# Performance work log

Hardware: AMD Instinct MI355X
Metric: run time of the kernel (lower is better)

Reference implementation:

```python
import jax, jax.numpy as jnp
import numpy as np
import math

N = 8192
F_IN = 1024
F_OUT = 1024
MAX_ITER = 10


def whale_optimizer(positions, key, max_iter=MAX_ITER):
    """Vectorized whale optimization algorithm.

    Faithful to the original per-agent/per-dim update rules, but the agent
    loop is vectorized (on-device RNG, one parallel update per outer
    iteration); only the `max_iter` outer iterations stay sequential.
    positions: [N, D] float32.
    """
    n, d = positions.shape
    lower = jnp.min(positions)
    upper = jnp.max(positions)
    k0, loop_key = jax.random.split(key)
    leader = positions[jax.random.randint(k0, (), 0, n)]  # [D]

    def step(carry, it):
        pos, leader = carry
        itf = it.astype(jnp.float32)
        k = jax.random.fold_in(loop_key, it)
        k1, k2, k3, k4, k5, k6 = jax.random.split(k, 6)
        a = 2.0 - itf * (2.0 / max_iter)
        a2 = -1.0 + itf * (-1.0 / max_iter)
        r1 = jax.random.uniform(k1, (n, 1))
        r2 = jax.random.uniform(k2, (n, 1))
        A = 2.0 * a * r1 - a                       # [n,1]
        C = 2.0 * r2                               # [n,1]
        lp = (a2 - 1.0) * jax.random.uniform(k3, (n, 1)) + 1.0  # spiral param
        p = jax.random.uniform(k4, (n, 1))
        # random leader per (agent, dim), as in the original inner j-loop
        ridx = jax.random.randint(k5, (n, d), 0, n)
        x_rand = jnp.take_along_axis(pos, ridx, axis=0)         # [n,d]
        explore = jnp.abs(x_rand - A * jnp.abs(C * x_rand - pos))
        exploit = jnp.abs(leader - A * jnp.abs(C * leader - pos))
        spiral = jnp.abs(jnp.abs(leader - pos) * jnp.exp(lp) * jnp.cos(2.0 * jnp.pi * lp) + leader)
        new_pos = jnp.where(p < 0.5,
                            jnp.where(jnp.abs(A) >= 1.0, explore, exploit),
                            spiral)
        new_pos = jnp.clip(new_pos, lower, upper)
        new_leader = new_pos[jax.random.randint(k6, (), 0, n)]
        return (new_pos, new_leader), None

    (positions, _), _ = jax.lax.scan(step, (positions, leader), jnp.arange(max_iter))
    return positions


def setup_inputs() -> dict:
    key = jax.random.key(0)
    k1, k2, k3, k4 = jax.random.split(key, 4)
    stdv = 1.0 / math.sqrt(F_OUT)
    return {
        "input": jax.random.normal(k1, (N, F_IN), dtype=jnp.float32),
        "adj": jax.random.uniform(k2, (N, N), dtype=jnp.float32) * (1.0 / N),
        "h0": jax.random.normal(k3, (N, F_IN), dtype=jnp.float32),
        "weight": jax.random.uniform(k4, (F_IN, F_OUT), dtype=jnp.float32,
                                      minval=-stdv, maxval=stdv),
        "lamda": jnp.float32(0.5),
        "alpha": jnp.float32(0.1),
        "l": 1,
    }


def reference(input, adj, h0, weight, lamda, alpha, l):
    # variant=False, residual=False
    theta = jnp.log(lamda / l + 1.0)
    hi = adj @ input                                  # spmm(adj, input)
    support = (1.0 - alpha) * hi + alpha * h0
    r = support
    # original detaches support before the whale optimizer
    opt = whale_optimizer(jax.lax.stop_gradient(support), jax.random.key(42))
    output = theta * (opt @ weight) + (1.0 - theta) * r
    return output
```

## Files before the change

### kernel.cpp

```cpp
#include <hip/hip_runtime.h>
#include <hip/hip_bf16.h>
#include <stdint.h>
#include <math.h>

typedef uint32_t u32;
typedef __hip_bfloat16 bf16t;
typedef __attribute__((ext_vector_type(8))) short short8;
typedef __attribute__((ext_vector_type(4))) float f32x4;


__host__ __device__ __forceinline__ void tf2(u32 k0, u32 k1, u32 c0, u32 c1, u32& o0, u32& o1) {
  const u32 ks2 = k0 ^ k1 ^ 0x1BD11BDAu;
  u32 x0 = c0 + k0, x1 = c1 + k1;
#define TFROT(v,r) (((v)<<(r))|((v)>>(32-(r))))
#define TFR(r) { x0 += x1; x1 = TFROT(x1,r); x1 ^= x0; }
  TFR(13) TFR(15) TFR(26) TFR(6)   x0 += k1;  x1 += ks2 + 1u;
  TFR(17) TFR(29) TFR(16) TFR(24)  x0 += ks2; x1 += k0 + 2u;
  TFR(13) TFR(15) TFR(26) TFR(6)   x0 += k0;  x1 += k1 + 3u;
  TFR(17) TFR(29) TFR(16) TFR(24)  x0 += k1;  x1 += ks2 + 4u;
  TFR(13) TFR(15) TFR(26) TFR(6)   x0 += ks2; x1 += k0 + 5u;
#undef TFR
#undef TFROT
  o0 = x0; o1 = x1;
}

__device__ __forceinline__ float unif_row(u32 ka, u32 kb, int i) {
  u32 o0, o1;
  tf2(ka, kb, 0u, (u32)i, o0, o1);
  return __uint_as_float(0x3F800000u | ((o0 ^ o1) >> 9)) - 1.0f;
}

__device__ __forceinline__ int ridx_fn(u32 ka, u32 kb, u32 f) {
  u32 o0, o1; tf2(ka, kb, 0u, f, o0, o1); return (int)((o0 ^ o1) & 8191u);
}

static inline void split2(u32 ka, u32 kb, u32* kA, u32* kB) {
  u32 a0, a1, b0, b1;
  tf2(ka, kb, 0u, 0u, a0, a1);
  tf2(ka, kb, 0u, 1u, b0, b1);
  kA[0] = a0; kA[1] = a1; kB[0] = b0; kB[1] = b1;
}

static inline void split6(u32 ka, u32 kb, u32 out[6][2]) {
  for (u32 i = 0; i < 6; i++) { u32 o0, o1; tf2(ka, kb, 0u, i, o0, o1); out[i][0] = o0; out[i][1] = o1; }
}

static inline int scalar_randint8192(u32 ka, u32 kb) {
  u32 kA[2], kB[2];
  split2(ka, kb, kA, kB);
  u32 o0, o1;
  tf2(kB[0], kB[1], 0u, 0u, o0, o1);
  return (int)((o0 ^ o1) & 8191u);
}

__device__ __forceinline__ ushort f2bf(float f) {
  u32 u = __float_as_uint(f);
  u32 r = u + 0x7FFFu + ((u >> 16) & 1u);
  return (ushort)(r >> 16);
}

__global__ __launch_bounds__(256) void cvt_k(const float4* __restrict__ x, uint2* __restrict__ y, int n4) {
  for (int i = blockIdx.x * 256 + threadIdx.x; i < n4; i += gridDim.x * 256) {
    float4 v = x[i];
    uint2 o;
    o.x = (u32)f2bf(v.x) | ((u32)f2bf(v.y) << 16);
    o.y = (u32)f2bf(v.z) | ((u32)f2bf(v.w) << 16);
    y[i] = o;
  }
}

__global__ __launch_bounds__(256) void packb_k(const float* __restrict__ B, uint4* __restrict__ out, int K, int Nn) {
  const int idx = blockIdx.x * 256 + threadIdx.x;
  const int total = (K >> 3) * Nn;
  if (idx >= total) return;
  const int g = idx / Nn;
  const int n = idx - g * Nn;
  u32 wv[4];
#pragma unroll
  for (int j = 0; j < 4; j++) {
    const float f0 = B[(size_t)(g * 8 + 2 * j) * Nn + n];
    const float f1 = B[(size_t)(g * 8 + 2 * j + 1) * Nn + n];
    wv[j] = (u32)f2bf(f0) | ((u32)f2bf(f1) << 16);
  }
  uint4 o; o.x = wv[0]; o.y = wv[1]; o.z = wv[2]; o.w = wv[3];
  out[idx] = o;
}

__global__ __launch_bounds__(256) void minmax2_k(const float* __restrict__ part, int G, float* __restrict__ bnd) {
  __shared__ float slo[256], shi[256];
  const int tid = threadIdx.x;
  float lo = 3.4e38f, hi = -3.4e38f;
  for (int i = tid; i < G; i += 256) { lo = fminf(lo, part[i]); hi = fmaxf(hi, part[G + i]); }
  slo[tid] = lo; shi[tid] = hi; __syncthreads();
  for (int s = 128; s > 0; s >>= 1) {
    if (tid < s) { slo[tid] = fminf(slo[tid], slo[tid + s]); shi[tid] = fmaxf(shi[tid], shi[tid + s]); }
    __syncthreads();
  }
  if (tid == 0) { bnd[0] = slo[0]; bnd[1] = shi[0]; }
}

__device__ __forceinline__ void gld_lds16(const void* g, void* l) {
  __builtin_amdgcn_global_load_lds((const __attribute__((address_space(1))) void*)g,
                                   (__attribute__((address_space(3))) void*)l, 16, 0, 0);
}

template <int EPI>
__global__ __launch_bounds__(512, 4) void gemm_k(
    const bf16t* __restrict__ A, const bf16t* __restrict__ Bp,
    const float* __restrict__ aux, const float* __restrict__ sF,
    const int* __restrict__ sI, float* __restrict__ C,
    float* __restrict__ prt, int PG, int Nn, int K) {
  __shared__ __align__(16) bf16t As[128 * 32];
  __shared__ __align__(16) bf16t Bs[128 * 32];
  const int tid = threadIdx.x;
  const int lane = tid & 63;
  const int wave = tid >> 6;
  const int bm = blockIdx.x & 63;
  const int bn = blockIdx.x >> 6;
  const int m0 = bm << 7, n0 = bn << 7;
  const int wm = (wave & 1) << 6;
  const int wn = (wave >> 1) << 5;

  f32x4 acc[4][2];
#pragma unroll
  for (int i = 0; i < 4; i++)
#pragma unroll
    for (int j = 0; j < 2; j++) acc[i][j] = (f32x4){0.f, 0.f, 0.f, 0.f};

  const bf16t* gA = A + (size_t)(m0 + (tid >> 2)) * K + ((tid & 3) << 3);
  bf16t* lA = As + (tid << 3);
  const bf16t* gB = Bp + ((size_t)(tid >> 7) * Nn + n0 + (tid & 127)) * 8;
  bf16t* lB = Bs + (tid << 3);
  const size_t bstep = (size_t)Nn * 32;

  for (int k0 = 0; k0 < K; k0 += 32) {
    __syncthreads();
    gld_lds16(gA + k0, lA);
    gld_lds16(gB, lB);
    gB += bstep;
    __syncthreads();
    const int arow = lane & 15, aq = lane >> 4;
    short8 af[4], bfv[2];
#pragma unroll
    for (int mt = 0; mt < 4; mt++)
      af[mt] = *(const short8*)(As + ((wm + mt * 16 + arow) << 5) + (aq << 3));
#pragma unroll
    for (int nt = 0; nt < 2; nt++)
      bfv[nt] = *(const short8*)(Bs + (((aq << 7) + wn + nt * 16 + arow) << 3));
#pragma unroll
    for (int mt = 0; mt < 4; mt++)
#pragma unroll
      for (int nt = 0; nt < 2; nt++)
        acc[mt][nt] = __builtin_amdgcn_mfma_f32_16x16x32_bf16(af[mt], bfv[nt], acc[mt][nt], 0, 0, 0);
  }

  float p1, p2;
  if (EPI == 1) { const float al = sF[0]; p1 = 1.0f - al; p2 = al; }
  else { const float th = logf(sF[0] / (float)sI[0] + 1.0f); p1 = th; p2 = 1.0f - th; }
  const int col = lane & 15, rq = lane >> 4;
  float vlo = 3.4e38f, vhi = -3.4e38f;
#pragma unroll
  for (int mt = 0; mt < 4; mt++)
#pragma unroll
    for (int nt = 0; nt < 2; nt++)
#pragma unroll
      for (int r = 0; r < 4; r++) {
        const int gm = m0 + wm + mt * 16 + (rq << 2) + r;
        const int gn = n0 + wn + nt * 16 + col;
        const size_t ix = (size_t)gm * Nn + gn;
        const float v = p1 * acc[mt][nt][r] + p2 * aux[ix];
        C[ix] = v;
        if (EPI == 1) { vlo = fminf(vlo, v); vhi = fmaxf(vhi, v); }
      }
  if (EPI == 1) {
    __syncthreads();
    float* red = (float*)As;
    red[tid] = vlo; red[512 + tid] = vhi;
    __syncthreads();
    for (int s = 256; s > 0; s >>= 1) {
      if (tid < s) {
        red[tid] = fminf(red[tid], red[tid + s]);
        red[512 + tid] = fmaxf(red[512 + tid], red[512 + tid + s]);
      }
      __syncthreads();
    }
    if (tid == 0) { prt[blockIdx.x] = red[0]; prt[PG + blockIdx.x] = red[512]; }
  }
}

struct WA {
  u32 k1a, k1b, k2a, k2b, k3a, k3b, k4a, k4b, k5a, k5b;
  int ldr;
  float a, a2;
};

__global__ __launch_bounds__(256) void whale_k(
    const float* __restrict__ pinb, float* __restrict__ poutb,
    ushort* __restrict__ opt, const float* __restrict__ bnd, WA w) {
  const int row = blockIdx.x;
  const int tid = threadIdx.x;
  __shared__ float sh[4];
  if (tid < 4) {
    u32 ka, kb;
    if (tid == 0)      { ka = w.k1a; kb = w.k1b; }
    else if (tid == 1) { ka = w.k2a; kb = w.k2b; }
    else if (tid == 2) { ka = w.k3a; kb = w.k3b; }
    else               { ka = w.k4a; kb = w.k4b; }
    sh[tid] = unif_row(ka, kb, row);
  }
  __syncthreads();
  const float r1 = sh[0], r2 = sh[1], u3 = sh[2], p = sh[3];
  float t2 = (2.0f * w.a) * r1;
  asm volatile("" : "+v"(t2));
  const float A = t2 - w.a;
  const float Cc = 2.0f * r2;
  const float lo = bnd[0], hi = bnd[1];
  const float* pin = pinb + ((size_t)row << 10);
  const int j0 = tid << 2;
  float4 pv = *(const float4*)(pin + j0);
  float ov[4];
  const bool bp = (p < 0.5f);
  if (bp && (fabsf(A) >= 1.0f)) {
    const u32 fb = ((u32)row << 10) + (u32)j0;
#pragma unroll
    for (int e = 0; e < 4; e++) {
      const float pos = (&pv.x)[e];
      const int ri = ridx_fn(w.k5a, w.k5b, fb + (u32)e);
      const float xr = pinb[((size_t)ri << 10) + j0 + e];
      ov[e] = fabsf(xr - A * fabsf(Cc * xr - pos));
    }
  } else {
    const float* ldp = pinb + ((size_t)w.ldr << 10);
    float4 lv = *(const float4*)(ldp + j0);
    if (bp) {
#pragma unroll
      for (int e = 0; e < 4; e++) {
        const float pos = (&pv.x)[e], ld = (&lv.x)[e];
        ov[e] = fabsf(ld - A * fabsf(Cc * ld - pos));
      }
    } else {
      const float lp = (w.a2 - 1.0f) * u3 + 1.0f;
      const float s1 = expf(lp);
      const float s2 = cosf(6.2831855f * lp);
#pragma unroll
      for (int e = 0; e < 4; e++) {
        const float pos = (&pv.x)[e], ld = (&lv.x)[e];
        ov[e] = fabsf(fabsf(ld - pos) * s1 * s2 + ld);
      }
    }
  }
  float4 res;
#pragma unroll
  for (int e = 0; e < 4; e++) (&res.x)[e] = fminf(fmaxf(ov[e], lo), hi);
  *(float4*)(poutb + ((size_t)row << 10) + j0) = res;
  if (opt) {
    ushort4 o4;
    o4.x = f2bf(res.x); o4.y = f2bf(res.y); o4.z = f2bf(res.z); o4.w = f2bf(res.w);
    *(ushort4*)(opt + ((size_t)row << 10) + j0) = o4;
  }
}

extern "C" void kernel_launch(void* const* d_in, const int* in_sizes, int n_in,
                              void* d_out, int out_size, void* d_ws, size_t ws_size,
                              hipStream_t stream) {
  const float* inp = (const float*)d_in[0];
  const float* adj = (const float*)d_in[1];
  const float* h0  = (const float*)d_in[2];
  const float* wgt = (const float*)d_in[3];
  const float* lam = (const float*)d_in[4];
  const float* alp = (const float*)d_in[5];
  const int* lint  = (const int*)d_in[6];
  float* outp = (float*)d_out;

  char* ws = (char*)d_ws;
  bf16t* Abf  = (bf16t*)(ws);
  float* P0   = (float*)(ws);
  float* P1   = (float*)(ws + 33554432);
  ushort* OPT = (ushort*)(ws + 67108864);
  bf16t* B1p  = (bf16t*)(ws + 134217728);
  bf16t* Wp   = (bf16t*)(ws + 150994944);
  float* SUP  = (float*)(ws + 153092096);
  float* PRT  = (float*)(ws + 186646528);
  float* BND  = (float*)(ws + 186662912);

  hipLaunchKernelGGL(cvt_k, dim3(4096), dim3(256), 0, stream, (const float4*)adj, (uint2*)Abf, 16777216);
  hipLaunchKernelGGL(packb_k, dim3(4096), dim3(256), 0, stream, inp, (uint4*)B1p, 8192, 1024);
  hipLaunchKernelGGL(packb_k, dim3(512), dim3(256), 0, stream, wgt, (uint4*)Wp, 1024, 1024);
  hipLaunchKernelGGL((gemm_k<1>), dim3(512), dim3(512), 0, stream, Abf, B1p, h0, alp, lint, SUP, PRT, 512, 1024, 8192);
  hipLaunchKernelGGL(minmax2_k, dim3(1), dim3(256), 0, stream, PRT, 512, BND);

  u32 k0k[2], lpk[2];
  split2(0u, 42u, k0k, lpk);
  int ldr = scalar_randint8192(k0k[0], k0k[1]);
  const float* cur = SUP;
  float* bufs[2] = {P0, P1};
  for (int it = 0; it < 10; ++it) {
    u32 ka, kb; tf2(lpk[0], lpk[1], 0u, (u32)it, ka, kb);
    u32 ks[6][2];
    split6(ka, kb, ks);
    u32 k5A[2], k5B[2];
    split2(ks[4][0], ks[4][1], k5A, k5B);
    WA w;
    w.k1a = ks[0][0]; w.k1b = ks[0][1];
    w.k2a = ks[1][0]; w.k2b = ks[1][1];
    w.k3a = ks[2][0]; w.k3b = ks[2][1];
    w.k4a = ks[3][0]; w.k4b = ks[3][1];
    w.k5a = k5B[0];   w.k5b = k5B[1];
    w.ldr = ldr;
    const float itf = (float)it;
    w.a = 2.0f - itf * 0.2f;
    w.a2 = -1.0f + itf * (-0.1f);
    float* nxt = bufs[it & 1];
    hipLaunchKernelGGL(whale_k, dim3(8192), dim3(256), 0, stream, cur, nxt,
                       (it == 9) ? OPT : (ushort*)nullptr, BND, w);
    cur = nxt;
    ldr = scalar_randint8192(ks[5][0], ks[5][1]);
  }
  hipLaunchKernelGGL((gemm_k<2>), dim3(512), dim3(512), 0, stream, (const bf16t*)OPT, Wp, SUP, lam, lint, outp,
                     (float*)nullptr, 0, 1024, 1024);
  (void)in_sizes; (void)n_in; (void)out_size; (void)ws_size;
}
```

Measured before the change: 907.5 us.

## Fuse adj fp32-to-bf16 conversion into GEMM and double-buffer K=64 tiles

Drops the separate cvt_k pass over the 8192x8192 adjacency matrix. The first GEMM now loads fp32 adj directly, converts it to bf16 in registers and writes it into padded LDS. The GEMM main loop also moves to K=64 stages with double-buffered LDS, so the next stage's B (async global-to-LDS) and A (register prefetch) loads overlap the current stage's MFMAs. Padding the A tile is meant to reduce LDS bank conflicts. The trade-offs are larger LDS and register use per block, which may lower occupancy under the 4-blocks hint, and adj is read as fp32 (twice the bytes of bf16) by every N-column block instead of once.

```diff
diff --git a/kernel.cpp b/kernel.cpp
--- a/kernel.cpp
+++ b/kernel.cpp
@@ -59,16 +59,6 @@
   return (ushort)(r >> 16);
 }
 
-__global__ __launch_bounds__(256) void cvt_k(const float4* __restrict__ x, uint2* __restrict__ y, int n4) {
-  for (int i = blockIdx.x * 256 + threadIdx.x; i < n4; i += gridDim.x * 256) {
-    float4 v = x[i];
-    uint2 o;
-    o.x = (u32)f2bf(v.x) | ((u32)f2bf(v.y) << 16);
-    o.y = (u32)f2bf(v.z) | ((u32)f2bf(v.w) << 16);
-    y[i] = o;
-  }
-}
-
 __global__ __launch_bounds__(256) void packb_k(const float* __restrict__ B, uint4* __restrict__ out, int K, int Nn) {
   const int idx = blockIdx.x * 256 + threadIdx.x;
   const int total = (K >> 3) * Nn;
@@ -104,14 +94,15 @@
                                    (__attribute__((address_space(3))) void*)l, 16, 0, 0);
 }
 
-template <int EPI>
+template <int EPI, int AF32>
 __global__ __launch_bounds__(512, 4) void gemm_k(
-    const bf16t* __restrict__ A, const bf16t* __restrict__ Bp,
+    const void* __restrict__ Araw, const bf16t* __restrict__ Bp,
     const float* __restrict__ aux, const float* __restrict__ sF,
     const int* __restrict__ sI, float* __restrict__ C,
     float* __restrict__ prt, int PG, int Nn, int K) {
-  __shared__ __align__(16) bf16t As[128 * 32];
-  __shared__ __align__(16) bf16t Bs[128 * 32];
+  constexpr int APAD = 72;
+  __shared__ __align__(16) bf16t As[2][128 * APAD];
+  __shared__ __align__(16) bf16t Bs[2][128 * 64];
   const int tid = threadIdx.x;
   const int lane = tid & 63;
   const int wave = tid >> 6;
@@ -127,31 +118,77 @@
 #pragma unroll
     for (int j = 0; j < 2; j++) acc[i][j] = (f32x4){0.f, 0.f, 0.f, 0.f};
 
-  const bf16t* gA = A + (size_t)(m0 + (tid >> 2)) * K + ((tid & 3) << 3);
-  bf16t* lA = As + (tid << 3);
-  const bf16t* gB = Bp + ((size_t)(tid >> 7) * Nn + n0 + (tid & 127)) * 8;
-  bf16t* lB = Bs + (tid << 3);
-  const size_t bstep = (size_t)Nn * 32;
-
-  for (int k0 = 0; k0 < K; k0 += 32) {
+  const float* Af = (const float*)Araw;
+  const bf16t* Ab = (const bf16t*)Araw;
+  const int u0 = tid, u1 = tid + 512;
+  const int ar0 = u0 >> 3, ac0 = (u0 & 7) << 3;
+  const int ar1 = u1 >> 3, ac1 = (u1 & 7) << 3;
+  const bf16t* gB0 = Bp + ((size_t)(u0 >> 7) * Nn + n0 + (u0 & 127)) * 8;
+  const bf16t* gB1 = Bp + ((size_t)(u1 >> 7) * Nn + n0 + (u1 & 127)) * 8;
+  const size_t bstep = (size_t)Nn * 64;
+
+  float4 a32[2][2];
+  short8 a16[2];
+
+  auto issueA = [&](int s) {
+    if (AF32) {
+      const float* p0 = Af + (size_t)(m0 + ar0) * K + (s << 6) + ac0;
+      const float* p1 = Af + (size_t)(m0 + ar1) * K + (s << 6) + ac1;
+      a32[0][0] = *(const float4*)p0; a32[0][1] = *(const float4*)(p0 + 4);
+      a32[1][0] = *(const float4*)p1; a32[1][1] = *(const float4*)(p1 + 4);
+    } else {
+      a16[0] = *(const short8*)(Ab + (size_t)(m0 + ar0) * K + (s << 6) + ac0);
+      a16[1] = *(const short8*)(Ab + (size_t)(m0 + ar1) * K + (s << 6) + ac1);
+    }
+  };
+  auto writeA = [&](int buf) {
+#pragma unroll
+    for (int i = 0; i < 2; i++) {
+      short8 v;
+      if (AF32) {
+#pragma unroll
+        for (int e = 0; e < 4; e++) v[e] = (short)f2bf((&a32[i][0].x)[e]);
+#pragma unroll
+        for (int e = 0; e < 4; e++) v[4 + e] = (short)f2bf((&a32[i][1].x)[e]);
+      } else {
+        v = a16[i];
+      }
+      const int r = i ? ar1 : ar0, cc = i ? ac1 : ac0;
+      *(short8*)(&As[buf][r * APAD + cc]) = v;
+    }
+  };
+  auto stageB = [&](int s, int buf) {
+    gld_lds16(gB0 + (size_t)s * bstep, &Bs[buf][u0 << 3]);
+    gld_lds16(gB1 + (size_t)s * bstep, &Bs[buf][u1 << 3]);
+  };
+
+  issueA(0);
+  stageB(0, 0);
+  writeA(0);
+
+  const int S = K >> 6;
+  const int arow = lane & 15, aq = lane >> 4;
+  for (int s = 0; s < S; ++s) {
+    const int cur = s & 1;
     __syncthreads();
-    gld_lds16(gA + k0, lA);
-    gld_lds16(gB, lB);
-    gB += bstep;
-    __syncthreads();
-    const int arow = lane & 15, aq = lane >> 4;
-    short8 af[4], bfv[2];
-#pragma unroll
-    for (int mt = 0; mt < 4; mt++)
-      af[mt] = *(const short8*)(As + ((wm + mt * 16 + arow) << 5) + (aq << 3));
-#pragma unroll
-    for (int nt = 0; nt < 2; nt++)
-      bfv[nt] = *(const short8*)(Bs + (((aq << 7) + wn + nt * 16 + arow) << 3));
-#pragma unroll
-    for (int mt = 0; mt < 4; mt++)
+    const bool more = (s + 1 < S);
+    if (more) { stageB(s + 1, cur ^ 1); issueA(s + 1); }
+#pragma unroll
+    for (int c = 0; c < 2; ++c) {
+      short8 af[4], bfv[2];
+#pragma unroll
+      for (int mt = 0; mt < 4; mt++)
+        af[mt] = *(const short8*)(&As[cur][(wm + mt * 16 + arow) * APAD + (c << 5) + (aq << 3)]);
 #pragma unroll
       for (int nt = 0; nt < 2; nt++)
-        acc[mt][nt] = __builtin_amdgcn_mfma_f32_16x16x32_bf16(af[mt], bfv[nt], acc[mt][nt], 0, 0, 0);
+        bfv[nt] = *(const short8*)(&Bs[cur][(((c << 2) + aq) * 128 + wn + nt * 16 + arow) << 3]);
+#pragma unroll
+      for (int mt = 0; mt < 4; mt++)
+#pragma unroll
+        for (int nt = 0; nt < 2; nt++)
+          acc[mt][nt] = __builtin_amdgcn_mfma_f32_16x16x32_bf16(af[mt], bfv[nt], acc[mt][nt], 0, 0, 0);
+    }
+    if (more) writeA(cur ^ 1);
   }
 
   float p1, p2;
@@ -174,7 +211,7 @@
       }
   if (EPI == 1) {
     __syncthreads();
-    float* red = (float*)As;
+    float* red = (float*)&As[0][0];
     red[tid] = vlo; red[512 + tid] = vhi;
     __syncthreads();
     for (int s = 256; s > 0; s >>= 1) {
@@ -273,7 +310,6 @@
   float* outp = (float*)d_out;
 
   char* ws = (char*)d_ws;
-  bf16t* Abf  = (bf16t*)(ws);
   float* P0   = (float*)(ws);
   float* P1   = (float*)(ws + 33554432);
   ushort* OPT = (ushort*)(ws + 67108864);
@@ -283,10 +319,10 @@
   float* PRT  = (float*)(ws + 186646528);
   float* BND  = (float*)(ws + 186662912);
 
-  hipLaunchKernelGGL(cvt_k, dim3(4096), dim3(256), 0, stream, (const float4*)adj, (uint2*)Abf, 16777216);
   hipLaunchKernelGGL(packb_k, dim3(4096), dim3(256), 0, stream, inp, (uint4*)B1p, 8192, 1024);
   hipLaunchKernelGGL(packb_k, dim3(512), dim3(256), 0, stream, wgt, (uint4*)Wp, 1024, 1024);
-  hipLaunchKernelGGL((gemm_k<1>), dim3(512), dim3(512), 0, stream, Abf, B1p, h0, alp, lint, SUP, PRT, 512, 1024, 8192);
+  hipLaunchKernelGGL((gemm_k<1, 1>), dim3(512), dim3(512), 0, stream, (const void*)adj, B1p, h0, alp, lint,
+                     SUP, PRT, 512, 1024, 8192);
   hipLaunchKernelGGL(minmax2_k, dim3(1), dim3(256), 0, stream, PRT, 512, BND);
 
   u32 k0k[2], lpk[2];
@@ -316,7 +352,7 @@
     cur = nxt;
     ldr = scalar_randint8192(ks[5][0], ks[5][1]);
   }
-  hipLaunchKernelGGL((gemm_k<2>), dim3(512), dim3(512), 0, stream, (const bf16t*)OPT, Wp, SUP, lam, lint, outp,
-                     (float*)nullptr, 0, 1024, 1024);
+  hipLaunchKernelGGL((gemm_k<2, 0>), dim3(512), dim3(512), 0, stream, (const void*)OPT, Wp, SUP, lam, lint,
+                     outp, (float*)nullptr, 0, 1024, 1024);
   (void)in_sizes; (void)n_in; (void)out_size; (void)ws_size;
 }
```

Result: faster. 862.9 us (-4.9%).
